# Optimization experiments

Hardware: AMD Instinct MI355X
Metric: run time of the kernel (lower is better)

Reference implementation:

```python
import jax, jax.numpy as jnp
import numpy as np

# dims
M, C, D = 64, 2000, 512          # clients, classes, embed_dim
H = 4                             # num_heads
HD = D // H                       # head_dim = 128
DFF = 2048                        # torch TransformerEncoderLayer default dim_feedforward
NUM_CLASSES = 2000
EPS = 1e-5


def _ln(x, g, b):
    mu = jnp.mean(x, axis=-1, keepdims=True)
    var = jnp.mean(jnp.square(x - mu), axis=-1, keepdims=True)
    return (x - mu) * jax.lax.rsqrt(var + EPS) * g + b


def setup_inputs() -> dict:
    key = jax.random.key(0)
    ks = jax.random.split(key, 16)
    s = 0.02
    return {
        "client_protos": jax.random.normal(ks[0], (M, C, D), jnp.float32),
        "norm_g": jnp.ones((D,), jnp.float32),
        "norm_b": jnp.zeros((D,), jnp.float32),
        "in_proj_w": jax.random.normal(ks[1], (3 * D, D), jnp.float32) * s,
        "in_proj_b": jnp.zeros((3 * D,), jnp.float32),
        "out_proj_w": jax.random.normal(ks[2], (D, D), jnp.float32) * s,
        "out_proj_b": jnp.zeros((D,), jnp.float32),
        "lin1_w": jax.random.normal(ks[3], (DFF, D), jnp.float32) * s,
        "lin1_b": jnp.zeros((DFF,), jnp.float32),
        "lin2_w": jax.random.normal(ks[4], (D, DFF), jnp.float32) * s,
        "lin2_b": jnp.zeros((D,), jnp.float32),
        "norm1_g": jnp.ones((D,), jnp.float32),
        "norm1_b": jnp.zeros((D,), jnp.float32),
        "norm2_g": jnp.ones((D,), jnp.float32),
        "norm2_b": jnp.zeros((D,), jnp.float32),
        "global_query": jax.random.normal(ks[5], (NUM_CLASSES, D), jnp.float32),
        "all_labels": jax.random.randint(ks[6], (C,), 0, NUM_CLASSES, jnp.int32),
        "round_num": 10,
        "client_idx": 0,
    }


def reference(client_protos, norm_g, norm_b, in_proj_w, in_proj_b,
              out_proj_w, out_proj_b, lin1_w, lin1_b, lin2_w, lin2_b,
              norm1_g, norm1_b, norm2_g, norm2_b, global_query,
              all_labels, round_num, client_idx):
    # 1) LayerNorm over all prototypes: (M, C, D)
    x = _ln(client_protos, norm_g, norm_b)
    # 2) Per-class transformer: original loops c in range(C) on (1, M, D).
    #    Batched: treat C as batch -> (C, M, D). Post-norm torch encoder layer.
    x = jnp.transpose(x, (1, 0, 2))  # (C, M, D)
    # self-attention
    qkv = x @ in_proj_w.T + in_proj_b          # (C, M, 3D)
    q, k, v = jnp.split(qkv, 3, axis=-1)
    q = q.reshape(C, M, H, HD)
    k = k.reshape(C, M, H, HD)
    v = v.reshape(C, M, H, HD)
    scores = jnp.einsum('cqhd,ckhd->chqk', q, k) / np.sqrt(HD).astype(np.float32)
    attn = jax.nn.softmax(scores, axis=-1)
    sa = jnp.einsum('chqk,ckhd->cqhd', attn, v).reshape(C, M, D)
    sa = sa @ out_proj_w.T + out_proj_b
    x = _ln(x + sa, norm1_g, norm1_b)
    # feed-forward (relu, dropout = eval no-op)
    ff = jax.nn.relu(x @ lin1_w.T + lin1_b) @ lin2_w.T + lin2_b
    x = _ln(x + ff, norm2_g, norm2_b)           # (C, M, D) == protos_trans^T
    # 3) Cross-attention with per-class global query
    q_all = global_query[all_labels].reshape(C, H, HD)
    kv_all = x.reshape(C, M, H, HD)
    s2 = jnp.einsum('chd,cmhd->chm', q_all, kv_all) / np.sqrt(HD).astype(np.float32)
    w2 = jax.nn.softmax(s2, axis=-1)
    attn_out = jnp.einsum('chm,cmhd->chd', w2, kv_all).reshape(C, D)
    return attn_out
```

## Files before the change

### kernel.cpp

```cpp
#include <hip/hip_runtime.h>

typedef _Float16 f16;
typedef _Float16 half4 __attribute__((ext_vector_type(4)));
typedef _Float16 half8 __attribute__((ext_vector_type(8)));
typedef float f32x4 __attribute__((ext_vector_type(4)));

typedef __attribute__((address_space(1))) void* as1v;
typedef __attribute__((address_space(3))) void* as3v;

#define SCALE 0.08838834764831845f

static __device__ __forceinline__ f32x4 mfma16(half8 a, half8 b, f32x4 c){
  return __builtin_amdgcn_mfma_f32_16x16x32_f16(a, b, c, 0, 0, 0);
}

__global__ __launch_bounds__(256) void k_cvt(const float* __restrict__ src, f16* __restrict__ dst, int n){
  int i = (blockIdx.x * 256 + threadIdx.x) * 8;
  if (i >= n) return;
  float4 a = *(const float4*)(src + i);
  float4 b = *(const float4*)(src + i + 4);
  half8 h;
  h[0] = (f16)a.x; h[1] = (f16)a.y; h[2] = (f16)a.z; h[3] = (f16)a.w;
  h[4] = (f16)b.x; h[5] = (f16)b.y; h[6] = (f16)b.z; h[7] = (f16)b.w;
  *(half8*)(dst + i) = h;
}

__global__ __launch_bounds__(256) void k_ln0(const float* __restrict__ protos,
                                             const float* __restrict__ g,
                                             const float* __restrict__ bb,
                                             f16* __restrict__ xb, int c0){
  const int w = threadIdx.x >> 6, l = threadIdx.x & 63;
  const int q = blockIdx.x * 4 + w;
  const int cl = q >> 6, m = q & 63;
  const float* in = protos + ((size_t)m * 2000 + (size_t)(c0 + cl)) * 512;
  const int d0 = l * 8;
  float4 a = *(const float4*)(in + d0);
  float4 c = *(const float4*)(in + d0 + 4);
  float s  = a.x + a.y + a.z + a.w + c.x + c.y + c.z + c.w;
  float ss = a.x*a.x + a.y*a.y + a.z*a.z + a.w*a.w + c.x*c.x + c.y*c.y + c.z*c.z + c.w*c.w;
#pragma unroll
  for (int msk = 1; msk < 64; msk <<= 1){ s += __shfl_xor(s, msk); ss += __shfl_xor(ss, msk); }
  const float mu = s * (1.f/512.f);
  const float rs = rsqrtf(ss * (1.f/512.f) - mu*mu + 1e-5f);
  float4 g0 = *(const float4*)(g + d0),  g1 = *(const float4*)(g + d0 + 4);
  float4 b0 = *(const float4*)(bb + d0), b1 = *(const float4*)(bb + d0 + 4);
  half8 o;
  o[0] = (f16)((a.x - mu) * rs * g0.x + b0.x);
  o[1] = (f16)((a.y - mu) * rs * g0.y + b0.y);
  o[2] = (f16)((a.z - mu) * rs * g0.z + b0.z);
  o[3] = (f16)((a.w - mu) * rs * g0.w + b0.w);
  o[4] = (f16)((c.x - mu) * rs * g1.x + b1.x);
  o[5] = (f16)((c.y - mu) * rs * g1.y + b1.y);
  o[6] = (f16)((c.z - mu) * rs * g1.z + b1.z);
  o[7] = (f16)((c.w - mu) * rs * g1.w + b1.w);
  *(half8*)(xb + (size_t)q * 512 + d0) = o;
}

__global__ __launch_bounds__(256) void k_resln(const f16* __restrict__ t, const f16* __restrict__ skip,
                                               const float* __restrict__ g, const float* __restrict__ bb,
                                               f16* __restrict__ outp){
  const int w = threadIdx.x >> 6, l = threadIdx.x & 63;
  const size_t q = (size_t)blockIdx.x * 4 + w;
  const int d0 = l * 8;
  half8 tv = *(const half8*)(t + q * 512 + d0);
  half8 sk = *(const half8*)(skip + q * 512 + d0);
  float v0 = (float)tv[0] + (float)sk[0], v1 = (float)tv[1] + (float)sk[1];
  float v2 = (float)tv[2] + (float)sk[2], v3 = (float)tv[3] + (float)sk[3];
  float v4 = (float)tv[4] + (float)sk[4], v5 = (float)tv[5] + (float)sk[5];
  float v6 = (float)tv[6] + (float)sk[6], v7 = (float)tv[7] + (float)sk[7];
  float s  = v0+v1+v2+v3+v4+v5+v6+v7;
  float ss = v0*v0+v1*v1+v2*v2+v3*v3+v4*v4+v5*v5+v6*v6+v7*v7;
#pragma unroll
  for (int msk = 1; msk < 64; msk <<= 1){ s += __shfl_xor(s, msk); ss += __shfl_xor(ss, msk); }
  const float mu = s * (1.f/512.f);
  const float rs = rsqrtf(ss * (1.f/512.f) - mu*mu + 1e-5f);
  float4 g0 = *(const float4*)(g + d0),  g1 = *(const float4*)(g + d0 + 4);
  float4 b0 = *(const float4*)(bb + d0), b1 = *(const float4*)(bb + d0 + 4);
  half8 o;
  o[0] = (f16)((v0 - mu) * rs * g0.x + b0.x);
  o[1] = (f16)((v1 - mu) * rs * g0.y + b0.y);
  o[2] = (f16)((v2 - mu) * rs * g0.z + b0.z);
  o[3] = (f16)((v3 - mu) * rs * g0.w + b0.w);
  o[4] = (f16)((v4 - mu) * rs * g1.x + b1.x);
  o[5] = (f16)((v5 - mu) * rs * g1.y + b1.y);
  o[6] = (f16)((v6 - mu) * rs * g1.z + b1.z);
  o[7] = (f16)((v7 - mu) * rs * g1.w + b1.w);
  *(half8*)(outp + q * 512 + d0) = o;
}

#define GLL(gp, lp) __builtin_amdgcn_global_load_lds((as1v)(void*)(gp), (as3v)(lp), 16, 0, 0)

template<bool RELU>
__global__ __launch_bounds__(256, 1) void k_gemm(const f16* __restrict__ A, const f16* __restrict__ B,
                                                 const float* __restrict__ bias, f16* __restrict__ Cout,
                                                 int N, int K, int gn){
  extern __shared__ char smem_raw[];
  f16* lds = (f16*)smem_raw;

  const int t = threadIdx.x, w = t >> 6, l = t & 63;
  const int wr = w >> 1, wc = w & 1;

  const int nwg = gridDim.x;
  const int q8 = nwg >> 3, r8 = nwg & 7;
  const int xcd = blockIdx.x & 7, lidx = blockIdx.x >> 3;
  const int swz = (xcd < r8 ? xcd * (q8 + 1) : r8 * (q8 + 1) + (xcd - r8) * q8) + lidx;
  const int tm = swz / gn, tn = swz % gn;
  const size_t row0 = (size_t)tm * 256;
  const int col0 = tn * 256;

  f32x4 acc[8][8];
#pragma unroll
  for (int m = 0; m < 8; ++m)
#pragma unroll
    for (int n = 0; n < 8; ++n) acc[m][n] = (f32x4){0.f,0.f,0.f,0.f};

  const int srow = t >> 2;
  const int sslot = (t & 3) ^ ((t >> 2) & 3);
  const f16* gA = A + (row0 + (size_t)srow) * (size_t)K + sslot * 8;
  const f16* gB = B + ((size_t)col0 + (size_t)srow) * (size_t)K + sslot * 8;
  const int dst0 = t * 8;

  const int arow = (l & 15) * 32 + (((l >> 4) ^ (l & 3)) << 3);
  const int aoff = wr * 128 * 32 + arow;
  const int boff = 8192 + wc * 128 * 32 + arow;

  const int NT = K >> 5;

  auto stage = [&](int tile, int slot){
    f16* base = lds + slot * 16384;
    const size_t ko = (size_t)tile * 32;
#pragma unroll
    for (int r = 0; r < 4; ++r)
      GLL(gA + ko + (size_t)(r * 64) * K, base + r * 2048 + dst0);
#pragma unroll
    for (int r = 0; r < 4; ++r)
      GLL(gB + ko + (size_t)(r * 64) * K, base + 8192 + r * 2048 + dst0);
  };

  stage(0, 0); stage(1, 1);
  asm volatile("s_waitcnt vmcnt(8)" ::: "memory");
  __builtin_amdgcn_s_barrier();

  int rs = 0, ws = 2;
  for (int tk = 0; tk < NT; ++tk){
    if (tk + 2 < NT) stage(tk + 2, ws);
    __builtin_amdgcn_sched_barrier(0);
    const f16* sb = lds + rs * 16384;
    half8 af[8], bf[8];
#pragma unroll
    for (int m = 0; m < 8; ++m) af[m] = *(const half8*)(sb + aoff + m * 512);
#pragma unroll
    for (int n = 0; n < 8; ++n) bf[n] = *(const half8*)(sb + boff + n * 512);
    __builtin_amdgcn_s_setprio(1);
#pragma unroll
    for (int m = 0; m < 8; ++m)
#pragma unroll
      for (int n = 0; n < 8; ++n)
        acc[m][n] = mfma16(bf[n], af[m], acc[m][n]);
    __builtin_amdgcn_s_setprio(0);
    if (tk + 2 < NT)      { asm volatile("s_waitcnt vmcnt(8)" ::: "memory"); }
    else if (tk + 1 < NT) { asm volatile("s_waitcnt vmcnt(0)" ::: "memory"); }
    __builtin_amdgcn_s_barrier();
    rs = (rs == 2) ? 0 : rs + 1;
    ws = (ws == 2) ? 0 : ws + 1;
  }

#pragma unroll
  for (int n = 0; n < 8; ++n){
    const int c = col0 + wc * 128 + n * 16 + ((l >> 4) << 2);
    float4 b4 = *(const float4*)(bias + c);
#pragma unroll
    for (int m = 0; m < 8; ++m){
      const size_t r = row0 + (size_t)(wr * 128 + m * 16 + (l & 15));
      float v0 = acc[m][n][0] + b4.x;
      float v1 = acc[m][n][1] + b4.y;
      float v2 = acc[m][n][2] + b4.z;
      float v3 = acc[m][n][3] + b4.w;
      if (RELU){ v0 = fmaxf(v0, 0.f); v1 = fmaxf(v1, 0.f); v2 = fmaxf(v2, 0.f); v3 = fmaxf(v3, 0.f); }
      half4 h; h[0] = (f16)v0; h[1] = (f16)v1; h[2] = (f16)v2; h[3] = (f16)v3;
      *(half4*)&Cout[r * (size_t)N + c] = h;
    }
  }
}

__global__ __launch_bounds__(256) void k_attn(const f16* __restrict__ qkv, f16* __restrict__ sa){
  __shared__ __align__(16) f16 P[4][4096];
  __shared__ __align__(16) f16 VT[4][4096];
  const int cl = blockIdx.x;
  const int h = threadIdx.x >> 6, l = threadIdx.x & 63;
  const f16* base = qkv + (size_t)cl * 64 * 1536;
  const f16* Qp = base + h * 128;
  const f16* Kp = base + 512 + h * 128;
  const f16* Vp = base + 1024 + h * 128;

  f32x4 s[4][4];
#pragma unroll
  for (int x = 0; x < 4; ++x)
#pragma unroll
    for (int y = 0; y < 4; ++y) s[x][y] = (f32x4){0.f,0.f,0.f,0.f};
#pragma unroll
  for (int ks = 0; ks < 4; ++ks){
    half8 aq[4], bk[4];
#pragma unroll
    for (int x = 0; x < 4; ++x)
      aq[x] = *(const half8*)&Qp[(size_t)(x * 16 + (l & 15)) * 1536 + ks * 32 + (l >> 4) * 8];
#pragma unroll
    for (int y = 0; y < 4; ++y)
      bk[y] = *(const half8*)&Kp[(size_t)(y * 16 + (l & 15)) * 1536 + ks * 32 + (l >> 4) * 8];
#pragma unroll
    for (int x = 0; x < 4; ++x)
#pragma unroll
      for (int y = 0; y < 4; ++y)
        s[x][y] = mfma16(aq[x], bk[y], s[x][y]);
  }

  char* Pb = (char*)&P[h][0];
#pragma unroll
  for (int x = 0; x < 4; ++x){
#pragma unroll
    for (int j = 0; j < 4; ++j){
      float e0 = s[x][0][j] * SCALE;
      float e1 = s[x][1][j] * SCALE;
      float e2 = s[x][2][j] * SCALE;
      float e3 = s[x][3][j] * SCALE;
      float mx = fmaxf(fmaxf(e0, e1), fmaxf(e2, e3));
#pragma unroll
      for (int msk = 1; msk < 16; msk <<= 1) mx = fmaxf(mx, __shfl_xor(mx, msk));
      e0 = __expf(e0 - mx); e1 = __expf(e1 - mx); e2 = __expf(e2 - mx); e3 = __expf(e3 - mx);
      float sm = e0 + e1 + e2 + e3;
#pragma unroll
      for (int msk = 1; msk < 16; msk <<= 1) sm += __shfl_xor(sm, msk);
      const float inv = 1.f / sm;
      const int row = x * 16 + (l >> 4) * 4 + j;
      const int rb = row * 128 + (l & 15) * 2;
      const int rsw = (row & 7) << 4;
      *(f16*)(Pb + ((rb     ) ^ rsw)) = (f16)(e0 * inv);
      *(f16*)(Pb + ((rb + 32) ^ rsw)) = (f16)(e1 * inv);
      *(f16*)(Pb + ((rb + 64) ^ rsw)) = (f16)(e2 * inv);
      *(f16*)(Pb + ((rb + 96) ^ rsw)) = (f16)(e3 * inv);
    }
  }

  char* Vb = (char*)&VT[h][0];
#pragma unroll
  for (int dh = 0; dh < 2; ++dh){
#pragma unroll
    for (int it = 0; it < 8; ++it){
      const int chunk = it * 64 + l;
      const int m = chunk >> 3, dc = chunk & 7;
      half8 v = *(const half8*)&Vp[(size_t)m * 1536 + dh * 64 + dc * 8];
#pragma unroll
      for (int jj = 0; jj < 8; ++jj){
        const int dd = dc * 8 + jj;
        *(f16*)(Vb + ((dd * 128 + m * 2) ^ ((dd & 7) << 4))) = v[jj];
      }
    }
    __syncthreads();
#pragma unroll
    for (int x = 0; x < 4; ++x){
      const int ar = x * 16 + (l & 15);
      const int ab = ar * 128, sw = (ar & 7) << 4;
      half8 ap0 = *(const half8*)(Pb + ((ab + (l >> 4) * 16) ^ sw));
      half8 ap1 = *(const half8*)(Pb + ((ab + 64 + (l >> 4) * 16) ^ sw));
#pragma unroll
      for (int dt = 0; dt < 4; ++dt){
        const int vr = dt * 16 + (l & 15);
        const int vb = vr * 128, vsw = (vr & 7) << 4;
        half8 b0 = *(const half8*)(Vb + ((vb + (l >> 4) * 16) ^ vsw));
        half8 b1 = *(const half8*)(Vb + ((vb + 64 + (l >> 4) * 16) ^ vsw));
        f32x4 o = (f32x4){0.f,0.f,0.f,0.f};
        o = mfma16(ap0, b0, o);
        o = mfma16(ap1, b1, o);
#pragma unroll
        for (int j = 0; j < 4; ++j){
          const int mrow = x * 16 + (l >> 4) * 4 + j;
          const int dcol = dh * 64 + dt * 16 + (l & 15);
          sa[((size_t)cl * 64 + mrow) * 512 + h * 128 + dcol] = (f16)o[j];
        }
      }
    }
    __syncthreads();
  }
}

__global__ __launch_bounds__(256) void k_cross(const f16* __restrict__ z, const float* __restrict__ gq,
                                               const int* __restrict__ labels, float* __restrict__ out,
                                               int c0){
  const int cl = blockIdx.x;
  const int h = threadIdx.x >> 6, l = threadIdx.x & 63;
  const int cg = c0 + cl;
  const float* q = gq + (size_t)labels[cg] * 512 + h * 128;
  const f16* zb = z + (size_t)cl * 64 * 512 + h * 128;

  const f16* zr = zb + (size_t)l * 512;
  float s = 0.f;
#pragma unroll
  for (int d = 0; d < 128; d += 8){
    half8 v = *(const half8*)&zr[d];
    float4 q0 = *(const float4*)&q[d];
    float4 q1 = *(const float4*)&q[d + 4];
    s += q0.x*(float)v[0] + q0.y*(float)v[1] + q0.z*(float)v[2] + q0.w*(float)v[3]
       + q1.x*(float)v[4] + q1.y*(float)v[5] + q1.z*(float)v[6] + q1.w*(float)v[7];
  }
  s *= SCALE;
  float mx = s;
#pragma unroll
  for (int msk = 1; msk < 64; msk <<= 1) mx = fmaxf(mx, __shfl_xor(mx, msk));
  float e = __expf(s - mx);
  float sm = e;
#pragma unroll
  for (int msk = 1; msk < 64; msk <<= 1) sm += __shfl_xor(sm, msk);
  const float wgt = e / sm;

  float a0 = 0.f, a1 = 0.f;
  for (int m = 0; m < 64; ++m){
    const float wm = __shfl(wgt, m);
    const f16* zm = zb + (size_t)m * 512 + 2 * l;
    a0 += wm * (float)zm[0];
    a1 += wm * (float)zm[1];
  }
  float2 o; o.x = a0; o.y = a1;
  *(float2*)&out[(size_t)cg * 512 + h * 128 + 2 * l] = o;
}

extern "C" void kernel_launch(void* const* d_in, const int* in_sizes, int n_in,
                              void* d_out, int out_size, void* d_ws, size_t ws_size,
                              hipStream_t stream){
  (void)in_sizes; (void)n_in; (void)out_size;
  const float* protos = (const float*)d_in[0];
  const float* norm_g = (const float*)d_in[1];
  const float* norm_b = (const float*)d_in[2];
  const float* in_w   = (const float*)d_in[3];
  const float* in_b   = (const float*)d_in[4];
  const float* ow     = (const float*)d_in[5];
  const float* ob     = (const float*)d_in[6];
  const float* l1w    = (const float*)d_in[7];
  const float* l1b    = (const float*)d_in[8];
  const float* l2w    = (const float*)d_in[9];
  const float* l2b    = (const float*)d_in[10];
  const float* n1g    = (const float*)d_in[11];
  const float* n1b    = (const float*)d_in[12];
  const float* n2g    = (const float*)d_in[13];
  const float* n2b    = (const float*)d_in[14];
  const float* gq     = (const float*)d_in[15];
  const int*   labels = (const int*)d_in[16];
  float* out = (float*)d_out;

  char* p = (char*)d_ws;
  auto alloc = [&](size_t bytes)->char*{
    char* r = p; p += (bytes + 255) & ~(size_t)255; return r;
  };
  f16* Wq = (f16*)alloc((size_t)1536*512*2);
  f16* Wo = (f16*)alloc((size_t)512*512*2);
  f16* W1 = (f16*)alloc((size_t)2048*512*2);
  f16* W2 = (f16*)alloc((size_t)512*2048*2);
  const size_t fixed = (size_t)(p - (char*)d_ws);

  const size_t per_class = (size_t)64*512*2 + (size_t)64*2048*2 + (size_t)64*512*2 + (size_t)64*512*2;
  long long avail = (long long)ws_size - (long long)fixed - 8192;
  long long cc_max = avail > 0 ? avail / (long long)per_class : 0;
  int Cc = (int)(cc_max > 2000 ? 2000 : cc_max);
  Cc &= ~3;
  if (Cc < 4) Cc = 4;

  f16* xb  = (f16*)alloc((size_t)Cc*64*512*2);
  f16* big = (f16*)alloc((size_t)Cc*64*2048*2);
  f16* sac = (f16*)alloc((size_t)Cc*64*512*2);
  f16* tmp = (f16*)alloc((size_t)Cc*64*512*2);

  k_cvt<<<1536*512/2048, 256, 0, stream>>>(in_w, Wq, 1536*512);
  k_cvt<<<512*512/2048,  256, 0, stream>>>(ow,   Wo, 512*512);
  k_cvt<<<2048*512/2048, 256, 0, stream>>>(l1w,  W1, 2048*512);
  k_cvt<<<2048*512/2048, 256, 0, stream>>>(l2w,  W2, 512*2048);

  const size_t SMEM = 98304;
  for (int c0 = 0; c0 < 2000; c0 += Cc){
    const int cc = (2000 - c0 < Cc) ? (2000 - c0) : Cc;
    const int R = cc * 64;
    const int gm = R / 256;
    k_ln0<<<R/4, 256, 0, stream>>>(protos, norm_g, norm_b, xb, c0);
    k_gemm<false><<<gm*6, 256, SMEM, stream>>>(xb, Wq, in_b, big, 1536, 512, 6);
    k_attn<<<cc, 256, 0, stream>>>(big, sac);
    k_gemm<false><<<gm*2, 256, SMEM, stream>>>(sac, Wo, ob, tmp, 512, 512, 2);
    k_resln<<<R/4, 256, 0, stream>>>(tmp, xb, n1g, n1b, sac);
    k_gemm<true><<<gm*8, 256, SMEM, stream>>>(sac, W1, l1b, big, 2048, 512, 8);
    k_gemm<false><<<gm*2, 256, SMEM, stream>>>(big, W2, l2b, tmp, 512, 2048, 2);
    k_resln<<<R/4, 256, 0, stream>>>(tmp, sac, n2g, n2b, big);
    k_cross<<<cc, 256, 0, stream>>>(big, gq, labels, out, c0);
  }
}
```

Baseline: 1.619 ms.

## Restructure GEMM to 8 waves with ping-pong register prefetch and split-phase loads

The GEMM kernel moves from 4 waves to 8 waves per 256x256 tile, each wave owning a 128x64 sub-tile, so accumulator registers are halved and two blocks can share a CU. The main loop is rewritten as a two-phase tile step. Global-to-LDS loads for A and B are issued in separate halves, and LDS fragment reads for the next tile are prefetched into ping-pong registers while MFMAs for the current tile run. The aim is to hide LDS and global latency and raise occupancy, at the cost of extra barriers, more complex waitcnt bookkeeping, and a new LDS swizzle that must match the load pattern.

```diff
diff --git a/kernel.cpp b/kernel.cpp
--- a/kernel.cpp
+++ b/kernel.cpp
@@ -90,15 +90,58 @@
 
 #define GLL(gp, lp) __builtin_amdgcn_global_load_lds((as1v)(void*)(gp), (as3v)(lp), 16, 0, 0)
 
+#define TILE_STEP(TT, BF, AF03, BFN, AF03N)                                     \
+{                                                                               \
+  const f16* sb = lds + rs * 16384;                                             \
+  f16* wb = lds + (rs >= 1 ? rs - 1 : 2) * 16384;                 \
+  const bool more2 = (TT) + 2 < NT;                                             \
+  const size_t ko2 = (size_t)((TT) + 2) * 32;                                   \
+     \
+  asm volatile("s_waitcnt lgkmcnt(0)" ::: "memory");                            \
+  __builtin_amdgcn_sched_barrier(0);                                            \
+  if (more2){ GLL(gA + ko2, wb + dst); GLL(gA + ko2 + half128, wb + 4096 + dst); } \
+  half8 af47[4];                                                                \
+  _Pragma("unroll") for (int m = 0; m < 4; ++m)                                 \
+    af47[m] = *(const half8*)(sb + aoff + (m + 4) * 512);                       \
+  __builtin_amdgcn_sched_barrier(0);                                            \
+  __builtin_amdgcn_s_setprio(1);                                                \
+  _Pragma("unroll") for (int m = 0; m < 4; ++m)                                 \
+    _Pragma("unroll") for (int n = 0; n < 4; ++n)                               \
+      acc[m][n] = mfma16(BF[n], AF03[m], acc[m][n]);                            \
+  __builtin_amdgcn_s_setprio(0);                                                \
+  if (more2)              { asm volatile("s_waitcnt vmcnt(2)" ::: "memory"); }  \
+  else if ((TT) + 1 < NT) { asm volatile("s_waitcnt vmcnt(0)" ::: "memory"); }  \
+  __builtin_amdgcn_s_barrier();                                                 \
+   \
+  asm volatile("s_waitcnt lgkmcnt(0)" ::: "memory");                            \
+  __builtin_amdgcn_sched_barrier(0);                                            \
+  if (more2){ GLL(gB + ko2, wb + 8192 + dst); GLL(gB + ko2 + half128, wb + 12288 + dst); } \
+  if ((TT) + 1 < NT){                                                           \
+    const f16* nb = lds + (rs == 2 ? 0 : rs + 1) * 16384;                       \
+    _Pragma("unroll") for (int n = 0; n < 4; ++n)                               \
+      BFN[n] = *(const half8*)(nb + boff + n * 512);                            \
+    _Pragma("unroll") for (int m = 0; m < 4; ++m)                               \
+      AF03N[m] = *(const half8*)(nb + aoff + m * 512);                          \
+  }                                                                             \
+  __builtin_amdgcn_sched_barrier(0);                                            \
+  __builtin_amdgcn_s_setprio(1);                                                \
+  _Pragma("unroll") for (int m = 0; m < 4; ++m)                                 \
+    _Pragma("unroll") for (int n = 0; n < 4; ++n)                               \
+      acc[m + 4][n] = mfma16(BF[n], af47[m], acc[m + 4][n]);                    \
+  __builtin_amdgcn_s_setprio(0);                                                \
+  __builtin_amdgcn_s_barrier();                                                 \
+  rs = (rs == 2) ? 0 : rs + 1;                                                  \
+}
+
 template<bool RELU>
-__global__ __launch_bounds__(256, 1) void k_gemm(const f16* __restrict__ A, const f16* __restrict__ B,
+__global__ __launch_bounds__(512, 2) void k_gemm(const f16* __restrict__ A, const f16* __restrict__ B,
                                                  const float* __restrict__ bias, f16* __restrict__ Cout,
                                                  int N, int K, int gn){
   extern __shared__ char smem_raw[];
   f16* lds = (f16*)smem_raw;
 
-  const int t = threadIdx.x, w = t >> 6, l = t & 63;
-  const int wr = w >> 1, wc = w & 1;
+  const int tid = threadIdx.x, w = tid >> 6, l = tid & 63;
+  const int wr = w >> 2, wc = w & 3;
 
   const int nwg = gridDim.x;
   const int q8 = nwg >> 3, r8 = nwg & 7;
@@ -108,66 +151,50 @@
   const size_t row0 = (size_t)tm * 256;
   const int col0 = tn * 256;
 
-  f32x4 acc[8][8];
+  f32x4 acc[8][4];
 #pragma unroll
   for (int m = 0; m < 8; ++m)
 #pragma unroll
-    for (int n = 0; n < 8; ++n) acc[m][n] = (f32x4){0.f,0.f,0.f,0.f};
-
-  const int srow = t >> 2;
-  const int sslot = (t & 3) ^ ((t >> 2) & 3);
-  const f16* gA = A + (row0 + (size_t)srow) * (size_t)K + sslot * 8;
-  const f16* gB = B + ((size_t)col0 + (size_t)srow) * (size_t)K + sslot * 8;
-  const int dst0 = t * 8;
-
-  const int arow = (l & 15) * 32 + (((l >> 4) ^ (l & 3)) << 3);
-  const int aoff = wr * 128 * 32 + arow;
-  const int boff = 8192 + wc * 128 * 32 + arow;
+    for (int n = 0; n < 4; ++n) acc[m][n] = (f32x4){0.f,0.f,0.f,0.f};
+
+  const int srcswz = ((tid & 3) ^ ((tid >> 3) & 3)) * 8;
+  const f16* gA = A + (row0 + (size_t)(tid >> 2)) * (size_t)K + srcswz;
+  const f16* gB = B + ((size_t)col0 + (size_t)(tid >> 2)) * (size_t)K + srcswz;
+  const int dst = tid * 8;
+  const size_t half128 = (size_t)128 * K;
+
+  const int psl = (((l >> 4) ^ ((l >> 1) & 3)) << 3);
+  const int aoff = (wr * 128 + (l & 15)) * 32 + psl;
+  const int boff = 8192 + (wc * 64 + (l & 15)) * 32 + psl;
 
   const int NT = K >> 5;
 
-  auto stage = [&](int tile, int slot){
-    f16* base = lds + slot * 16384;
-    const size_t ko = (size_t)tile * 32;
-#pragma unroll
-    for (int r = 0; r < 4; ++r)
-      GLL(gA + ko + (size_t)(r * 64) * K, base + r * 2048 + dst0);
-#pragma unroll
-    for (int r = 0; r < 4; ++r)
-      GLL(gB + ko + (size_t)(r * 64) * K, base + 8192 + r * 2048 + dst0);
-  };
-
-  stage(0, 0); stage(1, 1);
-  asm volatile("s_waitcnt vmcnt(8)" ::: "memory");
+  GLL(gA,                 lds + dst);
+  GLL(gA + half128,       lds + 4096 + dst);
+  GLL(gB,                 lds + 8192 + dst);
+  GLL(gB + half128,       lds + 12288 + dst);
+  GLL(gA + 32,            lds + 16384 + dst);
+  GLL(gA + 32 + half128,  lds + 16384 + 4096 + dst);
+  GLL(gB + 32,            lds + 16384 + 8192 + dst);
+  GLL(gB + 32 + half128,  lds + 16384 + 12288 + dst);
+  asm volatile("s_waitcnt vmcnt(4)" ::: "memory");
   __builtin_amdgcn_s_barrier();
 
-  int rs = 0, ws = 2;
-  for (int tk = 0; tk < NT; ++tk){
-    if (tk + 2 < NT) stage(tk + 2, ws);
-    __builtin_amdgcn_sched_barrier(0);
-    const f16* sb = lds + rs * 16384;
-    half8 af[8], bf[8];
-#pragma unroll
-    for (int m = 0; m < 8; ++m) af[m] = *(const half8*)(sb + aoff + m * 512);
-#pragma unroll
-    for (int n = 0; n < 8; ++n) bf[n] = *(const half8*)(sb + boff + n * 512);
-    __builtin_amdgcn_s_setprio(1);
-#pragma unroll
-    for (int m = 0; m < 8; ++m)
-#pragma unroll
-      for (int n = 0; n < 8; ++n)
-        acc[m][n] = mfma16(bf[n], af[m], acc[m][n]);
-    __builtin_amdgcn_s_setprio(0);
-    if (tk + 2 < NT)      { asm volatile("s_waitcnt vmcnt(8)" ::: "memory"); }
-    else if (tk + 1 < NT) { asm volatile("s_waitcnt vmcnt(0)" ::: "memory"); }
-    __builtin_amdgcn_s_barrier();
-    rs = (rs == 2) ? 0 : rs + 1;
-    ws = (ws == 2) ? 0 : ws + 1;
-  }
-
-#pragma unroll
-  for (int n = 0; n < 8; ++n){
-    const int c = col0 + wc * 128 + n * 16 + ((l >> 4) << 2);
+  half8 bf[4], af03[4], bfN[4], af03N[4];
+#pragma unroll
+  for (int n = 0; n < 4; ++n) bf[n] = *(const half8*)(lds + boff + n * 512);
+#pragma unroll
+  for (int m = 0; m < 4; ++m) af03[m] = *(const half8*)(lds + aoff + m * 512);
+
+  int rs = 0;
+  for (int t = 0; t < NT; t += 2){
+    TILE_STEP(t,     bf,  af03,  bfN, af03N)
+    TILE_STEP(t + 1, bfN, af03N, bf,  af03)
+  }
+
+#pragma unroll
+  for (int n = 0; n < 4; ++n){
+    const int c = col0 + wc * 64 + n * 16 + ((l >> 4) << 2);
     float4 b4 = *(const float4*)(bias + c);
 #pragma unroll
     for (int m = 0; m < 8; ++m){
@@ -379,12 +406,12 @@
     const int R = cc * 64;
     const int gm = R / 256;
     k_ln0<<<R/4, 256, 0, stream>>>(protos, norm_g, norm_b, xb, c0);
-    k_gemm<false><<<gm*6, 256, SMEM, stream>>>(xb, Wq, in_b, big, 1536, 512, 6);
+    k_gemm<false><<<gm*6, 512, SMEM, stream>>>(xb, Wq, in_b, big, 1536, 512, 6);
     k_attn<<<cc, 256, 0, stream>>>(big, sac);
-    k_gemm<false><<<gm*2, 256, SMEM, stream>>>(sac, Wo, ob, tmp, 512, 512, 2);
+    k_gemm<false><<<gm*2, 512, SMEM, stream>>>(sac, Wo, ob, tmp, 512, 512, 2);
     k_resln<<<R/4, 256, 0, stream>>>(tmp, xb, n1g, n1b, sac);
-    k_gemm<true><<<gm*8, 256, SMEM, stream>>>(sac, W1, l1b, big, 2048, 512, 8);
-    k_gemm<false><<<gm*2, 256, SMEM, stream>>>(big, W2, l2b, tmp, 512, 2048, 2);
+    k_gemm<true><<<gm*8, 512, SMEM, stream>>>(sac, W1, l1b, big, 2048, 512, 8);
+    k_gemm<false><<<gm*2, 512, SMEM, stream>>>(big, W2, l2b, tmp, 512, 2048, 2);
     k_resln<<<R/4, 256, 0, stream>>>(tmp, sac, n2g, n2b, big);
     k_cross<<<cc, 256, 0, stream>>>(big, gq, labels, out, c0);
   }
```

After: 1.574 ms. -2.8%, faster.

## Restructure GEMM to 8 waves with K=64 double buffer and interleaved load/compute phases

Applied to the files above, without the earlier changes.

The 256x256 tile GEMM moves from 4 waves with a 3-stage K=32 buffer to 8 waves (512 threads) with a double-buffered K=64 tile in 128KB LDS. Each iteration is split into four compute quadrants, and each quadrant issues part of the next tile's global-to-LDS loads, in the style of a ping-pong schedule. The goal is to raise MFMA issue density and hide load latency with more waves and fewer accumulators per wave. The cost is many more barriers per iteration and a larger LDS footprint. The launch bound of (512,2) cannot actually give two blocks per CU at 128KB LDS each.

```diff
diff --git a/kernel.cpp b/kernel.cpp
--- a/kernel.cpp
+++ b/kernel.cpp
@@ -91,14 +91,14 @@
 #define GLL(gp, lp) __builtin_amdgcn_global_load_lds((as1v)(void*)(gp), (as3v)(lp), 16, 0, 0)
 
 template<bool RELU>
-__global__ __launch_bounds__(256, 1) void k_gemm(const f16* __restrict__ A, const f16* __restrict__ B,
+__global__ __launch_bounds__(512, 2) void k_gemm(const f16* __restrict__ A, const f16* __restrict__ B,
                                                  const float* __restrict__ bias, f16* __restrict__ Cout,
                                                  int N, int K, int gn){
   extern __shared__ char smem_raw[];
   f16* lds = (f16*)smem_raw;
 
   const int t = threadIdx.x, w = t >> 6, l = t & 63;
-  const int wr = w >> 1, wc = w & 1;
+  const int wr = w >> 2, wc = w & 3;
 
   const int nwg = gridDim.x;
   const int q8 = nwg >> 3, r8 = nwg & 7;
@@ -108,66 +108,138 @@
   const size_t row0 = (size_t)tm * 256;
   const int col0 = tn * 256;
 
-  f32x4 acc[8][8];
+  f32x4 acc[8][4];
 #pragma unroll
   for (int m = 0; m < 8; ++m)
 #pragma unroll
-    for (int n = 0; n < 8; ++n) acc[m][n] = (f32x4){0.f,0.f,0.f,0.f};
-
-  const int srow = t >> 2;
-  const int sslot = (t & 3) ^ ((t >> 2) & 3);
-  const f16* gA = A + (row0 + (size_t)srow) * (size_t)K + sslot * 8;
-  const f16* gB = B + ((size_t)col0 + (size_t)srow) * (size_t)K + sslot * 8;
-  const int dst0 = t * 8;
-
-  const int arow = (l & 15) * 32 + (((l >> 4) ^ (l & 3)) << 3);
-  const int aoff = wr * 128 * 32 + arow;
-  const int boff = 8192 + wc * 128 * 32 + arow;
-
-  const int NT = K >> 5;
-
-  auto stage = [&](int tile, int slot){
-    f16* base = lds + slot * 16384;
-    const size_t ko = (size_t)tile * 32;
-#pragma unroll
-    for (int r = 0; r < 4; ++r)
-      GLL(gA + ko + (size_t)(r * 64) * K, base + r * 2048 + dst0);
-#pragma unroll
-    for (int r = 0; r < 4; ++r)
-      GLL(gB + ko + (size_t)(r * 64) * K, base + 8192 + r * 2048 + dst0);
+    for (int n = 0; n < 4; ++n) acc[m][n] = (f32x4){0.f,0.f,0.f,0.f};
+
+  const int lsw = ((t & 7) ^ ((t >> 3) & 7)) * 8;
+  const f16* gAb = A + (row0 + (size_t)(t >> 3)) * (size_t)K + lsw;
+  const f16* gBb = B + ((size_t)col0 + (size_t)(t >> 3)) * (size_t)K + lsw;
+  const int t8 = t * 8;
+
+  const int rA  = (l & 15) * 64;
+  const int ps0 = (((l >> 4) ^ (l & 7)) << 3);
+  const int ps1 = (((4 + (l >> 4)) ^ (l & 7)) << 3);
+  const int abase = wr * 8192 + rA;
+  const int bbase = 16384 + wc * 4096 + rA;
+
+  const int NT = K >> 6;
+
+  auto stgA = [&](int tt, int h){
+    f16* d = lds + (tt & 1) * 32768 + h * 8192 + t8;
+    const f16* s = gAb + (size_t)(h * 128) * K + (size_t)tt * 64;
+    GLL(s, d);
+    GLL(s + (size_t)64 * K, d + 4096);
   };
-
-  stage(0, 0); stage(1, 1);
-  asm volatile("s_waitcnt vmcnt(8)" ::: "memory");
+  auto stgB = [&](int tt, int h){
+    f16* d = lds + (tt & 1) * 32768 + 16384 + h * 8192 + t8;
+    const f16* s = gBb + (size_t)(h * 128) * K + (size_t)tt * 64;
+    GLL(s, d);
+    GLL(s + (size_t)64 * K, d + 4096);
+  };
+
+  stgA(0, 0); stgA(0, 1); stgB(0, 0); stgB(0, 1);
+  if (NT > 1){
+    stgA(1, 0);
+    asm volatile("s_waitcnt vmcnt(2)" ::: "memory");
+  } else {
+    asm volatile("s_waitcnt vmcnt(0)" ::: "memory");
+  }
   __builtin_amdgcn_s_barrier();
 
-  int rs = 0, ws = 2;
-  for (int tk = 0; tk < NT; ++tk){
-    if (tk + 2 < NT) stage(tk + 2, ws);
+  for (int tt = 0; tt < NT; ++tt){
+    const f16* sb = lds + (tt & 1) * 32768;
+    const bool s1 = tt + 1 < NT, s2 = tt + 2 < NT;
+    half8 af03[4][2], af47[4][2], bf[4][2];
+
+#pragma unroll
+    for (int m = 0; m < 4; ++m){
+      af03[m][0] = *(const half8*)(sb + abase + m * 1024 + ps0);
+      af03[m][1] = *(const half8*)(sb + abase + m * 1024 + ps1);
+    }
+#pragma unroll
+    for (int n = 0; n < 2; ++n){
+      bf[n][0] = *(const half8*)(sb + bbase + n * 1024 + ps0);
+      bf[n][1] = *(const half8*)(sb + bbase + n * 1024 + ps1);
+    }
+    if (s1) stgA(tt + 1, 1);
+    __builtin_amdgcn_s_barrier();
+    asm volatile("s_waitcnt lgkmcnt(0)" ::: "memory");
     __builtin_amdgcn_sched_barrier(0);
-    const f16* sb = lds + rs * 16384;
-    half8 af[8], bf[8];
-#pragma unroll
-    for (int m = 0; m < 8; ++m) af[m] = *(const half8*)(sb + aoff + m * 512);
-#pragma unroll
-    for (int n = 0; n < 8; ++n) bf[n] = *(const half8*)(sb + boff + n * 512);
     __builtin_amdgcn_s_setprio(1);
 #pragma unroll
-    for (int m = 0; m < 8; ++m)
-#pragma unroll
-      for (int n = 0; n < 8; ++n)
-        acc[m][n] = mfma16(bf[n], af[m], acc[m][n]);
+    for (int ks = 0; ks < 2; ++ks)
+#pragma unroll
+      for (int m = 0; m < 4; ++m)
+#pragma unroll
+        for (int n = 0; n < 2; ++n)
+          acc[m][n] = mfma16(bf[n][ks], af03[m][ks], acc[m][n]);
     __builtin_amdgcn_s_setprio(0);
-    if (tk + 2 < NT)      { asm volatile("s_waitcnt vmcnt(8)" ::: "memory"); }
-    else if (tk + 1 < NT) { asm volatile("s_waitcnt vmcnt(0)" ::: "memory"); }
-    __builtin_amdgcn_s_barrier();
-    rs = (rs == 2) ? 0 : rs + 1;
-    ws = (ws == 2) ? 0 : ws + 1;
-  }
-
-#pragma unroll
-  for (int n = 0; n < 8; ++n){
-    const int c = col0 + wc * 128 + n * 16 + ((l >> 4) << 2);
+    __builtin_amdgcn_s_barrier();
+
+#pragma unroll
+    for (int n = 2; n < 4; ++n){
+      bf[n][0] = *(const half8*)(sb + bbase + n * 1024 + ps0);
+      bf[n][1] = *(const half8*)(sb + bbase + n * 1024 + ps1);
+    }
+    if (s1) stgB(tt + 1, 0);
+    __builtin_amdgcn_s_barrier();
+    asm volatile("s_waitcnt lgkmcnt(0)" ::: "memory");
+    __builtin_amdgcn_sched_barrier(0);
+    __builtin_amdgcn_s_setprio(1);
+#pragma unroll
+    for (int ks = 0; ks < 2; ++ks)
+#pragma unroll
+      for (int m = 0; m < 4; ++m)
+#pragma unroll
+        for (int n = 2; n < 4; ++n)
+          acc[m][n] = mfma16(bf[n][ks], af03[m][ks], acc[m][n]);
+    __builtin_amdgcn_s_setprio(0);
+    __builtin_amdgcn_s_barrier();
+
+#pragma unroll
+    for (int m = 0; m < 4; ++m){
+      af47[m][0] = *(const half8*)(sb + abase + (m + 4) * 1024 + ps0);
+      af47[m][1] = *(const half8*)(sb + abase + (m + 4) * 1024 + ps1);
+    }
+    if (s1) stgB(tt + 1, 1);
+    __builtin_amdgcn_s_barrier();
+    asm volatile("s_waitcnt lgkmcnt(0)" ::: "memory");
+    __builtin_amdgcn_sched_barrier(0);
+    __builtin_amdgcn_s_setprio(1);
+#pragma unroll
+    for (int ks = 0; ks < 2; ++ks)
+#pragma unroll
+      for (int m = 0; m < 4; ++m)
+#pragma unroll
+        for (int n = 0; n < 2; ++n)
+          acc[m + 4][n] = mfma16(bf[n][ks], af47[m][ks], acc[m + 4][n]);
+    __builtin_amdgcn_s_setprio(0);
+    __builtin_amdgcn_s_barrier();
+
+    if (s2) stgA(tt + 2, 0);
+    __builtin_amdgcn_s_barrier();
+    __builtin_amdgcn_s_setprio(1);
+#pragma unroll
+    for (int ks = 0; ks < 2; ++ks)
+#pragma unroll
+      for (int m = 0; m < 4; ++m)
+#pragma unroll
+        for (int n = 2; n < 4; ++n)
+          acc[m + 4][n] = mfma16(bf[n][ks], af47[m][ks], acc[m + 4][n]);
+    __builtin_amdgcn_s_setprio(0);
+    if (s1){
+      if (s2) { asm volatile("s_waitcnt vmcnt(2)" ::: "memory"); }
+      else    { asm volatile("s_waitcnt vmcnt(0)" ::: "memory"); }
+    }
+    __builtin_amdgcn_s_barrier();
+  }
+
+#pragma unroll
+  for (int n = 0; n < 4; ++n){
+    const int c = col0 + wc * 64 + n * 16 + ((l >> 4) << 2);
     float4 b4 = *(const float4*)(bias + c);
 #pragma unroll
     for (int m = 0; m < 8; ++m){
@@ -373,18 +445,18 @@
   k_cvt<<<2048*512/2048, 256, 0, stream>>>(l1w,  W1, 2048*512);
   k_cvt<<<2048*512/2048, 256, 0, stream>>>(l2w,  W2, 512*2048);
 
-  const size_t SMEM = 98304;
+  const size_t SMEM = 131072;
   for (int c0 = 0; c0 < 2000; c0 += Cc){
     const int cc = (2000 - c0 < Cc) ? (2000 - c0) : Cc;
     const int R = cc * 64;
     const int gm = R / 256;
     k_ln0<<<R/4, 256, 0, stream>>>(protos, norm_g, norm_b, xb, c0);
-    k_gemm<false><<<gm*6, 256, SMEM, stream>>>(xb, Wq, in_b, big, 1536, 512, 6);
+    k_gemm<false><<<gm*6, 512, SMEM, stream>>>(xb, Wq, in_b, big, 1536, 512, 6);
     k_attn<<<cc, 256, 0, stream>>>(big, sac);
-    k_gemm<false><<<gm*2, 256, SMEM, stream>>>(sac, Wo, ob, tmp, 512, 512, 2);
+    k_gemm<false><<<gm*2, 512, SMEM, stream>>>(sac, Wo, ob, tmp, 512, 512, 2);
     k_resln<<<R/4, 256, 0, stream>>>(tmp, xb, n1g, n1b, sac);
-    k_gemm<true><<<gm*8, 256, SMEM, stream>>>(sac, W1, l1b, big, 2048, 512, 8);
-    k_gemm<false><<<gm*2, 256, SMEM, stream>>>(big, W2, l2b, tmp, 512, 2048, 2);
+    k_gemm<true><<<gm*8, 512, SMEM, stream>>>(sac, W1, l1b, big, 2048, 512, 8);
+    k_gemm<false><<<gm*2, 512, SMEM, stream>>>(big, W2, l2b, tmp, 512, 2048, 2);
     k_resln<<<R/4, 256, 0, stream>>>(tmp, sac, n2g, n2b, big);
     k_cross<<<cc, 256, 0, stream>>>(big, gq, labels, out, c0);
   }
```

Measured after the change: 1.497 ms. -7.5%, faster.

## Restructure GEMM to 512 threads with B fragments loaded directly into registers

Applied to the files above, without the earlier changes.

Rewrites the GEMM kernel to use 8 waves (2x4) per 256x256 tile with K-step 64, double-buffering only the A tile in LDS while each wave loads its B fragments straight from global memory into registers, prefetched one step ahead. LDS drops to 64KB, and the launch bounds now target two blocks per CU to raise occupancy and overlap. It also caps the class chunk size at 512, which bounds workspace use and adds more chunk iterations. The trade-off is redundant B global loads across waves and tighter register budgets under the occupancy hint.

```diff
diff --git a/kernel.cpp b/kernel.cpp
--- a/kernel.cpp
+++ b/kernel.cpp
@@ -91,14 +91,14 @@
 #define GLL(gp, lp) __builtin_amdgcn_global_load_lds((as1v)(void*)(gp), (as3v)(lp), 16, 0, 0)
 
 template<bool RELU>
-__global__ __launch_bounds__(256, 1) void k_gemm(const f16* __restrict__ A, const f16* __restrict__ B,
+__global__ __launch_bounds__(512, 2) void k_gemm(const f16* __restrict__ A, const f16* __restrict__ B,
                                                  const float* __restrict__ bias, f16* __restrict__ Cout,
                                                  int N, int K, int gn){
   extern __shared__ char smem_raw[];
   f16* lds = (f16*)smem_raw;
 
   const int t = threadIdx.x, w = t >> 6, l = t & 63;
-  const int wr = w >> 1, wc = w & 1;
+  const int wr = w >> 2, wc = w & 3;
 
   const int nwg = gridDim.x;
   const int q8 = nwg >> 3, r8 = nwg & 7;
@@ -108,66 +108,87 @@
   const size_t row0 = (size_t)tm * 256;
   const int col0 = tn * 256;
 
-  f32x4 acc[8][8];
+  f32x4 acc[8][4];
 #pragma unroll
   for (int m = 0; m < 8; ++m)
 #pragma unroll
-    for (int n = 0; n < 8; ++n) acc[m][n] = (f32x4){0.f,0.f,0.f,0.f};
-
-  const int srow = t >> 2;
-  const int sslot = (t & 3) ^ ((t >> 2) & 3);
-  const f16* gA = A + (row0 + (size_t)srow) * (size_t)K + sslot * 8;
-  const f16* gB = B + ((size_t)col0 + (size_t)srow) * (size_t)K + sslot * 8;
-  const int dst0 = t * 8;
-
-  const int arow = (l & 15) * 32 + (((l >> 4) ^ (l & 3)) << 3);
-  const int aoff = wr * 128 * 32 + arow;
-  const int boff = 8192 + wc * 128 * 32 + arow;
-
-  const int NT = K >> 5;
-
-  auto stage = [&](int tile, int slot){
-    f16* base = lds + slot * 16384;
-    const size_t ko = (size_t)tile * 32;
-#pragma unroll
-    for (int r = 0; r < 4; ++r)
-      GLL(gA + ko + (size_t)(r * 64) * K, base + r * 2048 + dst0);
-#pragma unroll
-    for (int r = 0; r < 4; ++r)
-      GLL(gB + ko + (size_t)(r * 64) * K, base + 8192 + r * 2048 + dst0);
+    for (int n = 0; n < 4; ++n) acc[m][n] = (f32x4){0.f,0.f,0.f,0.f};
+
+  const int lsw = ((t & 7) ^ ((t >> 3) & 7)) * 8;
+  const f16* gAb = A + (row0 + (size_t)(t >> 3)) * (size_t)K + lsw;
+  const int t8 = t * 8;
+
+  const int rA  = (l & 15) * 64;
+  const int ps0 = (((l >> 4) ^ (l & 7)) << 3);
+  const int ps1 = (((4 + (l >> 4)) ^ (l & 7)) << 3);
+  const int abase = wr * 8192 + rA;
+
+  const f16* gBf = B + (size_t)(col0 + wc * 64 + (l & 15)) * (size_t)K + (l >> 4) * 8;
+
+  const int NT = K >> 6;
+
+  auto stgA = [&](int tt){
+    f16* d = lds + (tt & 1) * 16384 + t8;
+    const f16* s = gAb + (size_t)tt * 64;
+    GLL(s,                   d);
+    GLL(s + (size_t) 64 * K, d + 4096);
+    GLL(s + (size_t)128 * K, d + 8192);
+    GLL(s + (size_t)192 * K, d + 12288);
   };
 
-  stage(0, 0); stage(1, 1);
+  half8 bc[4][2], bn[4][2];
+
+  stgA(0);
+  __builtin_amdgcn_sched_barrier(0);
+#pragma unroll
+  for (int nf = 0; nf < 4; ++nf){
+    bc[nf][0] = *(const half8*)(gBf + (size_t)nf * 16 * K);
+    bc[nf][1] = *(const half8*)(gBf + (size_t)nf * 16 * K + 32);
+  }
+  __builtin_amdgcn_sched_barrier(0);
   asm volatile("s_waitcnt vmcnt(8)" ::: "memory");
   __builtin_amdgcn_s_barrier();
 
-  int rs = 0, ws = 2;
   for (int tk = 0; tk < NT; ++tk){
-    if (tk + 2 < NT) stage(tk + 2, ws);
+    const bool more = tk + 1 < NT;
+    if (more) stgA(tk + 1);
     __builtin_amdgcn_sched_barrier(0);
-    const f16* sb = lds + rs * 16384;
-    half8 af[8], bf[8];
-#pragma unroll
-    for (int m = 0; m < 8; ++m) af[m] = *(const half8*)(sb + aoff + m * 512);
-#pragma unroll
-    for (int n = 0; n < 8; ++n) bf[n] = *(const half8*)(sb + boff + n * 512);
-    __builtin_amdgcn_s_setprio(1);
-#pragma unroll
-    for (int m = 0; m < 8; ++m)
-#pragma unroll
-      for (int n = 0; n < 8; ++n)
-        acc[m][n] = mfma16(bf[n], af[m], acc[m][n]);
-    __builtin_amdgcn_s_setprio(0);
-    if (tk + 2 < NT)      { asm volatile("s_waitcnt vmcnt(8)" ::: "memory"); }
-    else if (tk + 1 < NT) { asm volatile("s_waitcnt vmcnt(0)" ::: "memory"); }
+    if (more){
+      const size_t ko = (size_t)(tk + 1) * 64;
+#pragma unroll
+      for (int nf = 0; nf < 4; ++nf){
+        bn[nf][0] = *(const half8*)(gBf + (size_t)nf * 16 * K + ko);
+        bn[nf][1] = *(const half8*)(gBf + (size_t)nf * 16 * K + ko + 32);
+      }
+    }
+    __builtin_amdgcn_sched_barrier(0);
+
+    const f16* sb = lds + (tk & 1) * 16384;
+#pragma unroll
+    for (int ks = 0; ks < 2; ++ks){
+      const int ps = ks ? ps1 : ps0;
+      half8 af[8];
+#pragma unroll
+      for (int m = 0; m < 8; ++m) af[m] = *(const half8*)(sb + abase + m * 1024 + ps);
+      __builtin_amdgcn_s_setprio(1);
+#pragma unroll
+      for (int m = 0; m < 8; ++m)
+#pragma unroll
+        for (int n = 0; n < 4; ++n)
+          acc[m][n] = mfma16(bc[n][ks], af[m], acc[m][n]);
+      __builtin_amdgcn_s_setprio(0);
+    }
+    if (more){
+#pragma unroll
+      for (int nf = 0; nf < 4; ++nf){ bc[nf][0] = bn[nf][0]; bc[nf][1] = bn[nf][1]; }
+      asm volatile("s_waitcnt vmcnt(8)" ::: "memory");
+    }
     __builtin_amdgcn_s_barrier();
-    rs = (rs == 2) ? 0 : rs + 1;
-    ws = (ws == 2) ? 0 : ws + 1;
-  }
-
-#pragma unroll
-  for (int n = 0; n < 8; ++n){
-    const int c = col0 + wc * 128 + n * 16 + ((l >> 4) << 2);
+  }
+
+#pragma unroll
+  for (int n = 0; n < 4; ++n){
+    const int c = col0 + wc * 64 + n * 16 + ((l >> 4) << 2);
     float4 b4 = *(const float4*)(bias + c);
 #pragma unroll
     for (int m = 0; m < 8; ++m){
@@ -360,6 +381,7 @@
   long long avail = (long long)ws_size - (long long)fixed - 8192;
   long long cc_max = avail > 0 ? avail / (long long)per_class : 0;
   int Cc = (int)(cc_max > 2000 ? 2000 : cc_max);
+  if (Cc > 512) Cc = 512;
   Cc &= ~3;
   if (Cc < 4) Cc = 4;
 
@@ -373,18 +395,18 @@
   k_cvt<<<2048*512/2048, 256, 0, stream>>>(l1w,  W1, 2048*512);
   k_cvt<<<2048*512/2048, 256, 0, stream>>>(l2w,  W2, 512*2048);
 
-  const size_t SMEM = 98304;
+  const size_t SMEM = 65536;
   for (int c0 = 0; c0 < 2000; c0 += Cc){
     const int cc = (2000 - c0 < Cc) ? (2000 - c0) : Cc;
     const int R = cc * 64;
     const int gm = R / 256;
     k_ln0<<<R/4, 256, 0, stream>>>(protos, norm_g, norm_b, xb, c0);
-    k_gemm<false><<<gm*6, 256, SMEM, stream>>>(xb, Wq, in_b, big, 1536, 512, 6);
+    k_gemm<false><<<gm*6, 512, SMEM, stream>>>(xb, Wq, in_b, big, 1536, 512, 6);
     k_attn<<<cc, 256, 0, stream>>>(big, sac);
-    k_gemm<false><<<gm*2, 256, SMEM, stream>>>(sac, Wo, ob, tmp, 512, 512, 2);
+    k_gemm<false><<<gm*2, 512, SMEM, stream>>>(sac, Wo, ob, tmp, 512, 512, 2);
     k_resln<<<R/4, 256, 0, stream>>>(tmp, xb, n1g, n1b, sac);
-    k_gemm<true><<<gm*8, 256, SMEM, stream>>>(sac, W1, l1b, big, 2048, 512, 8);
-    k_gemm<false><<<gm*2, 256, SMEM, stream>>>(big, W2, l2b, tmp, 512, 2048, 2);
+    k_gemm<true><<<gm*8, 512, SMEM, stream>>>(sac, W1, l1b, big, 2048, 512, 8);
+    k_gemm<false><<<gm*2, 512, SMEM, stream>>>(big, W2, l2b, tmp, 512, 2048, 2);
     k_resln<<<R/4, 256, 0, stream>>>(tmp, sac, n2g, n2b, big);
     k_cross<<<cc, 256, 0, stream>>>(big, gq, labels, out, c0);
   }
```

Measured after the change: 1.971 ms. 21.8% more time.
